# Kernel optimization log

Measured on AMD Instinct MI355X. Metric: run time of the kernel, lower is better.

The kernel has to match this reference:

```python
import jax, jax.numpy as jnp
import numpy as np

K = 3  # kernel_size
P = K * K  # patch length per channel


def setup_inputs() -> dict:
    key = jax.random.key(0)
    k1, k2 = jax.random.split(key)
    B, H, W, C_in, C_out = 16, 64, 64, 64, 64
    L = P * (P + 1) // 2 + P + 1  # 45 quadratic + 9 linear + 1 bias = 55
    x = jax.random.normal(k1, (B, H, W, C_in), dtype=jnp.float32)
    # glorot-ish scale for the flat kernel [1,1,L,C_in,C_out]
    flat_kernel = jax.random.normal(k2, (1, 1, L, C_in, C_out), dtype=jnp.float32) * 0.05
    return {"x": x, "flat_kernel": flat_kernel}


def _quadratic_features(x):
    # x: [B,H,W,C] NHWC; stride 1, 'same' padding, k=3
    B, H, W, C = x.shape
    pad = K // 2
    xp = jnp.pad(x, ((0, 0), (pad, pad), (pad, pad), (0, 0)))
    # patches: [B,H,W,P,C] -- loop is over the 9 fixed kernel taps only
    patches = jnp.stack(
        [xp[:, i:i + H, j:j + W, :] for i in range(K) for j in range(K)], axis=3
    )
    iu, ju = np.triu_indices(P)  # all pairs i<=j incl. squares -> 45 terms
    quad = patches[:, :, :, iu, :] * patches[:, :, :, ju, :]  # [B,H,W,45,C]
    ones = jnp.ones_like(patches[:, :, :, :1, :])              # bias term
    # flat features per the use_linear_and_bias=True layout: [quad | linear | 1]
    return jnp.concatenate([quad, patches, ones], axis=3)       # [B,H,W,55,C]


def reference(x, flat_kernel):
    feats = _quadratic_features(x)          # [B,H,W,L,C]
    w = flat_kernel[0, 0]                   # [L,C,O]
    # contract over flat-feature index L and input channels C
    return jnp.einsum('bhwlc,lco->bhwo', feats, w)
```

## Files before the change

### kernel.cpp

```cpp
#include <hip/hip_runtime.h>

typedef _Float16 half8 __attribute__((ext_vector_type(8)));
typedef _Float16 half4v __attribute__((ext_vector_type(4)));
typedef float f32x16 __attribute__((ext_vector_type(16)));

#define BOFF 0
#define XOFF 110592
#define LDS_TOTAL 152832

__device__ __forceinline__ void stage16(const void* g, const void* l) {
  __builtin_amdgcn_global_load_lds(
      (const __attribute__((address_space(1))) unsigned int*)(unsigned long long)g,
      (__attribute__((address_space(3))) unsigned int*)(unsigned int)(unsigned long long)l,
      16, 0, 0);
}

__global__ __launch_bounds__(256)
void prepack_kernel(const float* __restrict__ W, _Float16* __restrict__ Bp) {
  const int idx = blockIdx.x * 256 + threadIdx.x;
  if (idx < 221184) {
    const int v   = idx & 7;
    const int lam = (idx >> 3) & 63;
    const int f   = idx >> 9;
    const int l   = f % 54;
    const int r   = f / 54;
    const int cc  = r & 1;
    const int ks  = (r >> 1) & 1;
    const int nt  = (r >> 2) & 1;
    const int c   = (ks * 2 + cc) * 16 + (lam >> 5) * 8 + v;
    const int o   = nt * 32 + (lam & 31);
    Bp[idx] = (_Float16)W[(l * 64 + c) * 64 + o];
  } else if (idx < 221184 + 64) {
    const int o = idx - 221184;
    float s = 0.f;
    for (int c = 0; c < 64; ++c) s += W[(54 * 64 + c) * 64 + o];
    ((float*)(Bp + 221184))[o] = s;
  }
}

__global__ __launch_bounds__(512, 2)
void qconv_kernel(const float* __restrict__ x, const _Float16* __restrict__ Bp,
                  float* __restrict__ out) {
  constexpr int IU[45] = {0,0,0,0,0,0,0,0,0, 1,1,1,1,1,1,1,1, 2,2,2,2,2,2,2,
                          3,3,3,3,3,3, 4,4,4,4,4, 5,5,5,5, 6,6,6, 7,7, 8};
  constexpr int JU[45] = {0,1,2,3,4,5,6,7,8, 1,2,3,4,5,6,7,8, 2,3,4,5,6,7,8,
                          3,4,5,6,7,8, 4,5,6,7,8, 5,6,7,8, 6,7,8, 7,8, 8};

  const int tid  = threadIdx.x;
  const int wave = tid >> 6;
  const int lane = tid & 63;
  const int colA = lane & 31;
  const int kg   = lane >> 5;

  const int phys = blockIdx.x;
  const int xcd  = phys & 7;
  const int slot = phys >> 3;
  const int g    = xcd * 16 + (slot >> 1);
  const int nt   = slot & 1;
  const int b    = g >> 3;
  const int r0   = (g & 7) * 8;

  __shared__ __align__(16) unsigned char smem[LDS_TOTAL];
  const char* BpB = (const char*)Bp;

  f32x16 acc[2] = {};

  for (int ks = 0; ks < 2; ++ks) {
    __syncthreads();

    const size_t bSrc = (size_t)(nt * 2 + ks) * 110592;
    for (int f = wave; f < 108; f += 8)
      stage16(BpB + bSrc + (size_t)f * 1024 + lane * 16,
              (char*)smem + BOFF + f * 1024);

    for (int idx = tid; idx < 5280; idx += 512) {
      const int row = idx / 528;
      const int rem = idx - row * 528;
      const int col = rem >> 3;
      const int gq  = rem & 7;
      const int hh  = r0 - 1 + row;
      const int ww  = col - 1;
      float4 v = make_float4(0.f, 0.f, 0.f, 0.f);
      if ((unsigned)hh < 64u && (unsigned)ww < 64u)
        v = *(const float4*)(x + ((((size_t)b * 64 + hh) * 64 + ww) * 64
                                  + ks * 32 + gq * 4));
      half4v hv;
      hv[0] = (_Float16)v.x; hv[1] = (_Float16)v.y;
      hv[2] = (_Float16)v.z; hv[3] = (_Float16)v.w;
      const int addr = XOFF + ((row * 4224 + col * 64 + gq * 8)
                               ^ (((col >> 1) & 3) << 4));
      *(half4v*)(smem + addr) = hv;
    }

    asm volatile("s_waitcnt vmcnt(0)" ::: "memory");
    __syncthreads();

#pragma unroll
    for (int cc = 0; cc < 2; ++cc) {
      half8 tap[2][9];
#pragma unroll
      for (int mt = 0; mt < 2; ++mt)
#pragma unroll
        for (int t = 0; t < 9; ++t) {
          const int xrow = wave + t / 3;
          const int ce   = mt * 32 + colA + (t % 3);
          const int a = XOFF + ((xrow * 4224 + ce * 64 + cc * 32 + kg * 16)
                                ^ (((ce >> 1) & 3) << 4));
          tap[mt][t] = *(const half8*)(smem + a);
        }

      const unsigned fb = BOFF + cc * 54 * 1024 + lane * 16;
      half8 pfA = *(const half8*)(smem + fb);
      half8 pfB = *(const half8*)(smem + fb + 1024);
#pragma unroll
      for (int l = 0; l < 54; ++l) {
        const half8 bf = (l & 1) ? pfB : pfA;
        if (l + 2 < 54) {
          if (l & 1) pfB = *(const half8*)(smem + fb + (l + 2) * 1024);
          else       pfA = *(const half8*)(smem + fb + (l + 2) * 1024);
        }
#pragma unroll
        for (int mt = 0; mt < 2; ++mt) {
          half8 a;
          if (l < 45) a = tap[mt][IU[l]] * tap[mt][JU[l]];
          else        a = tap[mt][l - 45];
          acc[mt] = __builtin_amdgcn_mfma_f32_32x32x16_f16(a, bf, acc[mt],
                                                           0, 0, 0);
        }
      }
    }
  }

  const float bias = ((const float*)(BpB + 442368))[nt * 32 + colA];
#pragma unroll
  for (int mt = 0; mt < 2; ++mt) {
    float* op = out + (((size_t)b * 64 + r0 + wave) * 64 + mt * 32) * 64
                    + nt * 32 + colA;
#pragma unroll
    for (int gi = 0; gi < 16; ++gi) {
      const int rowD = (gi & 3) + 8 * (gi >> 2) + 4 * kg;
      op[(size_t)rowD * 64] = acc[mt][gi] + bias;
    }
  }
}

extern "C" void kernel_launch(void* const* d_in, const int* in_sizes, int n_in,
                              void* d_out, int out_size, void* d_ws, size_t ws_size,
                              hipStream_t stream) {
  const float* x = (const float*)d_in[0];
  const float* W = (const float*)d_in[1];
  float* out     = (float*)d_out;
  _Float16* Bp   = (_Float16*)d_ws;

  prepack_kernel<<<dim3((221248 + 255) / 256), dim3(256), 0, stream>>>(W, Bp);
  qconv_kernel<<<dim3(256), dim3(512), 0, stream>>>(x, Bp, out);
}
```

Baseline: 40.61 us.

## Double-buffer weight slices in LDS and load input taps directly from global

Splits the reduction into four channel-chunk phases, each staging only one 54-row weight slice into one of two LDS slots. The next slice is prefetched asynchronously while the current one is consumed, with a single barrier per phase. The LDS staging of the input halo tile is removed: each lane reads its 9 taps straight from global memory as float4 pairs and converts them to half in registers, and weight reads are prefetched eight deep. This cuts LDS use and barrier stalls, but adds redundant global reads of overlapping taps across lanes and waves, and more register pressure.

Result: slower. 61.58 us (+51.6%).

```diff
diff --git a/kernel.cpp b/kernel.cpp
--- a/kernel.cpp
+++ b/kernel.cpp
@@ -1,12 +1,10 @@
 #include <hip/hip_runtime.h>
 
 typedef _Float16 half8 __attribute__((ext_vector_type(8)));
-typedef _Float16 half4v __attribute__((ext_vector_type(4)));
 typedef float f32x16 __attribute__((ext_vector_type(16)));
 
-#define BOFF 0
-#define XOFF 110592
-#define LDS_TOTAL 152832
+#define SLOT 55296
+#define LDS_TOTAL (2 * SLOT)
 
 __device__ __forceinline__ void stage16(const void* g, const void* l) {
   __builtin_amdgcn_global_load_lds(
@@ -59,82 +57,97 @@
   const int nt   = slot & 1;
   const int b    = g >> 3;
   const int r0   = (g & 7) * 8;
+  const int r    = r0 + wave;
 
   __shared__ __align__(16) unsigned char smem[LDS_TOTAL];
   const char* BpB = (const char*)Bp;
 
+  {
+    const size_t src = (size_t)((nt * 2 + 0) * 2 + 0) * SLOT;
+#pragma unroll
+    for (int q = 0; q < 7; ++q) {
+      const int f = min(wave * 7 + q, 53);
+      stage16(BpB + src + (size_t)f * 1024 + lane * 16,
+              (char*)smem + 0 * SLOT + f * 1024);
+    }
+  }
+  __syncthreads();
+
   f32x16 acc[2] = {};
 
-  for (int ks = 0; ks < 2; ++ks) {
-    __syncthreads();
+  for (int p = 0; p < 4; ++p) {
+    const int ks = p >> 1;
+    const int cc = p & 1;
+    const int chb = (ks * 2 + cc) * 16 + kg * 8;
 
-    const size_t bSrc = (size_t)(nt * 2 + ks) * 110592;
-    for (int f = wave; f < 108; f += 8)
-      stage16(BpB + bSrc + (size_t)f * 1024 + lane * 16,
-              (char*)smem + BOFF + f * 1024);
-
-    for (int idx = tid; idx < 5280; idx += 512) {
-      const int row = idx / 528;
-      const int rem = idx - row * 528;
-      const int col = rem >> 3;
-      const int gq  = rem & 7;
-      const int hh  = r0 - 1 + row;
-      const int ww  = col - 1;
-      float4 v = make_float4(0.f, 0.f, 0.f, 0.f);
-      if ((unsigned)hh < 64u && (unsigned)ww < 64u)
-        v = *(const float4*)(x + ((((size_t)b * 64 + hh) * 64 + ww) * 64
-                                  + ks * 32 + gq * 4));
-      half4v hv;
-      hv[0] = (_Float16)v.x; hv[1] = (_Float16)v.y;
-      hv[2] = (_Float16)v.z; hv[3] = (_Float16)v.w;
-      const int addr = XOFF + ((row * 4224 + col * 64 + gq * 8)
-                               ^ (((col >> 1) & 3) << 4));
-      *(half4v*)(smem + addr) = hv;
+    half8 tap[2][9];
+#pragma unroll
+    for (int mt = 0; mt < 2; ++mt) {
+      float4 tlo[9], thi[9];
+#pragma unroll
+      for (int t = 0; t < 9; ++t) {
+        const int rr = r + t / 3 - 1;
+        const int cl = mt * 32 + colA + (t % 3) - 1;
+        float4 z = make_float4(0.f, 0.f, 0.f, 0.f);
+        tlo[t] = z; thi[t] = z;
+        if ((unsigned)rr < 64u && (unsigned)cl < 64u) {
+          const float* pa = x + ((((size_t)b * 64 + rr) * 64 + cl) * 64 + chb);
+          tlo[t] = *(const float4*)pa;
+          thi[t] = *(const float4*)(pa + 4);
+        }
+      }
+#pragma unroll
+      for (int t = 0; t < 9; ++t) {
+        half8 hv;
+        hv[0] = (_Float16)tlo[t].x; hv[1] = (_Float16)tlo[t].y;
+        hv[2] = (_Float16)tlo[t].z; hv[3] = (_Float16)tlo[t].w;
+        hv[4] = (_Float16)thi[t].x; hv[5] = (_Float16)thi[t].y;
+        hv[6] = (_Float16)thi[t].z; hv[7] = (_Float16)thi[t].w;
+        tap[mt][t] = hv;
+      }
     }
 
-    asm volatile("s_waitcnt vmcnt(0)" ::: "memory");
-    __syncthreads();
-
+    asm volatile("" ::: "memory");
+    if (p < 3) {
+      const int pn = p + 1;
+      const size_t src = (size_t)((nt * 2 + (pn >> 1)) * 2 + (pn & 1)) * SLOT;
 #pragma unroll
-    for (int cc = 0; cc < 2; ++cc) {
-      half8 tap[2][9];
-#pragma unroll
-      for (int mt = 0; mt < 2; ++mt)
-#pragma unroll
-        for (int t = 0; t < 9; ++t) {
-          const int xrow = wave + t / 3;
-          const int ce   = mt * 32 + colA + (t % 3);
-          const int a = XOFF + ((xrow * 4224 + ce * 64 + cc * 32 + kg * 16)
-                                ^ (((ce >> 1) & 3) << 4));
-          tap[mt][t] = *(const half8*)(smem + a);
-        }
-
-      const unsigned fb = BOFF + cc * 54 * 1024 + lane * 16;
-      half8 pfA = *(const half8*)(smem + fb);
-      half8 pfB = *(const half8*)(smem + fb + 1024);
-#pragma unroll
-      for (int l = 0; l < 54; ++l) {
-        const half8 bf = (l & 1) ? pfB : pfA;
-        if (l + 2 < 54) {
-          if (l & 1) pfB = *(const half8*)(smem + fb + (l + 2) * 1024);
-          else       pfA = *(const half8*)(smem + fb + (l + 2) * 1024);
-        }
-#pragma unroll
-        for (int mt = 0; mt < 2; ++mt) {
-          half8 a;
-          if (l < 45) a = tap[mt][IU[l]] * tap[mt][JU[l]];
-          else        a = tap[mt][l - 45];
-          acc[mt] = __builtin_amdgcn_mfma_f32_32x32x16_f16(a, bf, acc[mt],
-                                                           0, 0, 0);
-        }
+      for (int q = 0; q < 7; ++q) {
+        const int f = min(wave * 7 + q, 53);
+        stage16(BpB + src + (size_t)f * 1024 + lane * 16,
+                (char*)smem + (pn & 1) * SLOT + f * 1024);
       }
     }
+
+    const unsigned sbase = (p & 1) * SLOT + lane * 16;
+    half8 bq[8];
+#pragma unroll
+    for (int q = 0; q < 8; ++q)
+      bq[q] = *(const half8*)(smem + sbase + q * 1024);
+#pragma unroll
+    for (int l = 0; l < 54; ++l) {
+      const half8 bf = bq[l & 7];
+      if (l + 8 < 54)
+        bq[l & 7] = *(const half8*)(smem + sbase + (l + 8) * 1024);
+      half8 a0, a1;
+      if (l < 45) {
+        a0 = tap[0][IU[l]] * tap[0][JU[l]];
+        a1 = tap[1][IU[l]] * tap[1][JU[l]];
+      } else {
+        a0 = tap[0][l - 45];
+        a1 = tap[1][l - 45];
+      }
+      acc[0] = __builtin_amdgcn_mfma_f32_32x32x16_f16(a0, bf, acc[0], 0, 0, 0);
+      acc[1] = __builtin_amdgcn_mfma_f32_32x32x16_f16(a1, bf, acc[1], 0, 0, 0);
+    }
+
+    __syncthreads();
   }
 
   const float bias = ((const float*)(BpB + 442368))[nt * 32 + colA];
 #pragma unroll
   for (int mt = 0; mt < 2; ++mt) {
-    float* op = out + (((size_t)b * 64 + r0 + wave) * 64 + mt * 32) * 64
+    float* op = out + (((size_t)b * 64 + r) * 64 + mt * 32) * 64
                     + nt * 32 + colA;
 #pragma unroll
     for (int gi = 0; gi < 16; ++gi) {
```

## Software-pipeline LDS loads of weights and taps across MFMA groups

Applied to the files above, without the earlier changes.

Restructures the inner compute into groups of nine MFMA steps with double-buffered weight fragments loaded a group ahead. The second channel-chunk's tap loads are spread across the first chunk's MFMA groups, and s_setprio is raised around MFMA bursts. The aim is to hide LDS latency behind matrix ops. In exchange it holds many more live half8 values in registers, which risks spills under the 2-blocks-per-CU launch bound.

Result: slower. 55.96 us (+37.8%).

```diff
diff --git a/kernel.cpp b/kernel.cpp
--- a/kernel.cpp
+++ b/kernel.cpp
@@ -64,6 +64,54 @@
   const char* BpB = (const char*)Bp;
 
   f32x16 acc[2] = {};
+  half8 bqE[9], bqO[9];
+  half8 tapA[2][9], tapB[2][9];
+
+#define TAPLOAD(tp, cc)                                                     \
+  _Pragma("unroll")                                                         \
+  for (int mt = 0; mt < 2; ++mt)                                            \
+    _Pragma("unroll")                                                       \
+    for (int t = 0; t < 9; ++t) {                                           \
+      const int xrow = wave + t / 3;                                        \
+      const int ce   = mt * 32 + colA + (t % 3);                            \
+      const int aa = XOFF + ((xrow * 4224 + ce * 64 + (cc) * 32 + kg * 16)  \
+                             ^ (((ce >> 1) & 3) << 4));                     \
+      tp[mt][t] = *(const half8*)(smem + aa);                               \
+    }
+
+#define LOADQ(buf, cc, p)                                                   \
+  _Pragma("unroll")                                                         \
+  for (int q = 0; q < 9; ++q)                                               \
+    buf[q] = *(const half8*)(smem + BOFF + (cc) * 55296 +                   \
+                             ((p) * 9 + q) * 1024 + lane * 16);
+
+#define TRICK(p)                                                            \
+  _Pragma("unroll")                                                         \
+  for (int j = 0; j < 3; ++j) {                                             \
+    const int q  = (p) * 3 + j;                                             \
+    const int mt = q / 9, tt = q % 9;                                       \
+    const int xrow = wave + tt / 3;                                         \
+    const int ce   = mt * 32 + colA + (tt % 3);                             \
+    const int aa = XOFF + ((xrow * 4224 + ce * 64 + 32 + kg * 16)           \
+                           ^ (((ce >> 1) & 3) << 4));                       \
+    tapB[mt][tt] = *(const half8*)(smem + aa);                              \
+  }
+
+#define MFMA9(tp, buf, l0)                                                  \
+  __builtin_amdgcn_s_setprio(1);                                            \
+  _Pragma("unroll")                                                         \
+  for (int q = 0; q < 9; ++q) {                                             \
+    const int l = (l0) + q;                                                 \
+    half8 a0, a1;                                                           \
+    if (l < 45) { a0 = tp[0][IU[l]] * tp[0][JU[l]];                         \
+                  a1 = tp[1][IU[l]] * tp[1][JU[l]]; }                       \
+    else        { a0 = tp[0][l - 45]; a1 = tp[1][l - 45]; }                 \
+    acc[0] = __builtin_amdgcn_mfma_f32_32x32x16_f16(a0, buf[q], acc[0],     \
+                                                    0, 0, 0);               \
+    acc[1] = __builtin_amdgcn_mfma_f32_32x32x16_f16(a1, buf[q], acc[1],     \
+                                                    0, 0, 0);               \
+  }                                                                         \
+  __builtin_amdgcn_s_setprio(0);
 
   for (int ks = 0; ks < 2; ++ks) {
     __syncthreads();
@@ -95,40 +143,20 @@
     asm volatile("s_waitcnt vmcnt(0)" ::: "memory");
     __syncthreads();
 
-#pragma unroll
-    for (int cc = 0; cc < 2; ++cc) {
-      half8 tap[2][9];
-#pragma unroll
-      for (int mt = 0; mt < 2; ++mt)
-#pragma unroll
-        for (int t = 0; t < 9; ++t) {
-          const int xrow = wave + t / 3;
-          const int ce   = mt * 32 + colA + (t % 3);
-          const int a = XOFF + ((xrow * 4224 + ce * 64 + cc * 32 + kg * 16)
-                                ^ (((ce >> 1) & 3) << 4));
-          tap[mt][t] = *(const half8*)(smem + a);
-        }
-
-      const unsigned fb = BOFF + cc * 54 * 1024 + lane * 16;
-      half8 pfA = *(const half8*)(smem + fb);
-      half8 pfB = *(const half8*)(smem + fb + 1024);
-#pragma unroll
-      for (int l = 0; l < 54; ++l) {
-        const half8 bf = (l & 1) ? pfB : pfA;
-        if (l + 2 < 54) {
-          if (l & 1) pfB = *(const half8*)(smem + fb + (l + 2) * 1024);
-          else       pfA = *(const half8*)(smem + fb + (l + 2) * 1024);
-        }
-#pragma unroll
-        for (int mt = 0; mt < 2; ++mt) {
-          half8 a;
-          if (l < 45) a = tap[mt][IU[l]] * tap[mt][JU[l]];
-          else        a = tap[mt][l - 45];
-          acc[mt] = __builtin_amdgcn_mfma_f32_32x32x16_f16(a, bf, acc[mt],
-                                                           0, 0, 0);
-        }
-      }
-    }
+    TAPLOAD(tapA, 0);
+    LOADQ(bqE, 0, 0);
+    LOADQ(bqO, 0, 1);  TRICK(0);  MFMA9(tapA, bqE, 0);
+    LOADQ(bqE, 0, 2);  TRICK(1);  MFMA9(tapA, bqO, 9);
+    LOADQ(bqO, 0, 3);  TRICK(2);  MFMA9(tapA, bqE, 18);
+    LOADQ(bqE, 0, 4);  TRICK(3);  MFMA9(tapA, bqO, 27);
+    LOADQ(bqO, 0, 5);  TRICK(4);  MFMA9(tapA, bqE, 36);
+    LOADQ(bqE, 1, 0);  TRICK(5);  MFMA9(tapA, bqO, 45);
+    LOADQ(bqO, 1, 1);  MFMA9(tapB, bqE, 0);
+    LOADQ(bqE, 1, 2);  MFMA9(tapB, bqO, 9);
+    LOADQ(bqO, 1, 3);  MFMA9(tapB, bqE, 18);
+    LOADQ(bqE, 1, 4);  MFMA9(tapB, bqO, 27);
+    LOADQ(bqO, 1, 5);  MFMA9(tapB, bqE, 36);
+                       MFMA9(tapB, bqO, 45);
   }
 
   const float bias = ((const float*)(BpB + 442368))[nt * 32 + colA];
```

## Halve block size, stage weights per channel chunk, and batch LDS loads around MFMA groups

Applied to the files above, without the earlier changes.

The grid doubles to 512 blocks of 256 threads, each covering 4 output rows instead of 8, and LDS use drops to about 80 KB so two blocks can share a CU. Weights are now staged one 32-channel chunk at a time across four phases instead of two. The x tile is reloaded only when the input-channel half changes. The inner loop loads weight fragments in groups of six, double-buffered, and raises wave priority around each MFMA burst to overlap LDS reads with matrix work. The cost is more barriers and global weight traffic per output row, plus a larger halo overhead from the smaller row tiles.

Result: slower. 42.33 us (+4.2%).

```diff
diff --git a/kernel.cpp b/kernel.cpp
--- a/kernel.cpp
+++ b/kernel.cpp
@@ -5,8 +5,8 @@
 typedef float f32x16 __attribute__((ext_vector_type(16)));
 
 #define BOFF 0
-#define XOFF 110592
-#define LDS_TOTAL 152832
+#define XOFF 55296
+#define LDS_TOTAL 80640
 
 __device__ __forceinline__ void stage16(const void* g, const void* l) {
   __builtin_amdgcn_global_load_lds(
@@ -38,7 +38,7 @@
   }
 }
 
-__global__ __launch_bounds__(512, 2)
+__global__ __launch_bounds__(256, 2)
 void qconv_kernel(const float* __restrict__ x, const _Float16* __restrict__ Bp,
                   float* __restrict__ out) {
   constexpr int IU[45] = {0,0,0,0,0,0,0,0,0, 1,1,1,1,1,1,1,1, 2,2,2,2,2,2,2,
@@ -53,88 +53,102 @@
   const int kg   = lane >> 5;
 
   const int phys = blockIdx.x;
-  const int xcd  = phys & 7;
-  const int slot = phys >> 3;
-  const int g    = xcd * 16 + (slot >> 1);
-  const int nt   = slot & 1;
-  const int b    = g >> 3;
-  const int r0   = (g & 7) * 8;
+  const int logical = (phys & 7) * 64 + (phys >> 3);
+  const int nt  = logical & 1;
+  const int grp = logical >> 1;
+  const int b   = grp >> 4;
+  const int r0  = (grp & 15) * 4;
+  const int r   = r0 + wave;
 
   __shared__ __align__(16) unsigned char smem[LDS_TOTAL];
   const char* BpB = (const char*)Bp;
 
   f32x16 acc[2] = {};
+  half8 tap[2][9];
+  half8 bqE[6], bqO[6];
 
-  for (int ks = 0; ks < 2; ++ks) {
+#define LOADQ(buf, p)                                                       \
+  _Pragma("unroll")                                                         \
+  for (int q = 0; q < 6; ++q)                                               \
+    buf[q] = *(const half8*)(smem + BOFF + ((p) * 6 + q) * 1024 + lane * 16);
+
+#define MFMA6(buf, l0)                                                      \
+  __builtin_amdgcn_s_setprio(1);                                            \
+  _Pragma("unroll")                                                         \
+  for (int q = 0; q < 6; ++q) {                                             \
+    const int l = (l0) + q;                                                 \
+    half8 a0, a1;                                                           \
+    if (l < 45) { a0 = tap[0][IU[l]] * tap[0][JU[l]];                       \
+                  a1 = tap[1][IU[l]] * tap[1][JU[l]]; }                     \
+    else        { a0 = tap[0][l - 45]; a1 = tap[1][l - 45]; }               \
+    acc[0] = __builtin_amdgcn_mfma_f32_32x32x16_f16(a0, buf[q], acc[0],     \
+                                                    0, 0, 0);               \
+    acc[1] = __builtin_amdgcn_mfma_f32_32x32x16_f16(a1, buf[q], acc[1],     \
+                                                    0, 0, 0);               \
+  }                                                                         \
+  __builtin_amdgcn_s_setprio(0);
+
+  for (int p = 0; p < 4; ++p) {
+    const int ks = p >> 1;
+    const int cc = p & 1;
     __syncthreads();
 
-    const size_t bSrc = (size_t)(nt * 2 + ks) * 110592;
-    for (int f = wave; f < 108; f += 8)
-      stage16(BpB + bSrc + (size_t)f * 1024 + lane * 16,
+    const size_t bsrc = (size_t)(((nt * 2 + ks) * 2 + cc) * 54) * 1024;
+    for (int f = wave; f < 54; f += 4)
+      stage16(BpB + bsrc + (size_t)f * 1024 + lane * 16,
               (char*)smem + BOFF + f * 1024);
 
-    for (int idx = tid; idx < 5280; idx += 512) {
-      const int row = idx / 528;
-      const int rem = idx - row * 528;
-      const int col = rem >> 3;
-      const int gq  = rem & 7;
-      const int hh  = r0 - 1 + row;
-      const int ww  = col - 1;
-      float4 v = make_float4(0.f, 0.f, 0.f, 0.f);
-      if ((unsigned)hh < 64u && (unsigned)ww < 64u)
-        v = *(const float4*)(x + ((((size_t)b * 64 + hh) * 64 + ww) * 64
-                                  + ks * 32 + gq * 4));
-      half4v hv;
-      hv[0] = (_Float16)v.x; hv[1] = (_Float16)v.y;
-      hv[2] = (_Float16)v.z; hv[3] = (_Float16)v.w;
-      const int addr = XOFF + ((row * 4224 + col * 64 + gq * 8)
-                               ^ (((col >> 1) & 3) << 4));
-      *(half4v*)(smem + addr) = hv;
+    if (cc == 0) {
+      for (int idx = tid; idx < 3168; idx += 256) {
+        const int row = idx / 528;
+        const int rem = idx - row * 528;
+        const int col = rem >> 3;
+        const int gq  = rem & 7;
+        const int hh  = r0 - 1 + row;
+        const int ww  = col - 1;
+        float4 v = make_float4(0.f, 0.f, 0.f, 0.f);
+        if ((unsigned)hh < 64u && (unsigned)ww < 64u)
+          v = *(const float4*)(x + ((((size_t)b * 64 + hh) * 64 + ww) * 64
+                                    + ks * 32 + gq * 4));
+        half4v hv;
+        hv[0] = (_Float16)v.x; hv[1] = (_Float16)v.y;
+        hv[2] = (_Float16)v.z; hv[3] = (_Float16)v.w;
+        const int addr = XOFF + ((row * 4224 + col * 64 + gq * 8)
+                                 ^ (((col >> 1) & 3) << 4));
+        *(half4v*)(smem + addr) = hv;
+      }
     }
 
     asm volatile("s_waitcnt vmcnt(0)" ::: "memory");
     __syncthreads();
 
 #pragma unroll
-    for (int cc = 0; cc < 2; ++cc) {
-      half8 tap[2][9];
+    for (int mt = 0; mt < 2; ++mt)
 #pragma unroll
-      for (int mt = 0; mt < 2; ++mt)
-#pragma unroll
-        for (int t = 0; t < 9; ++t) {
-          const int xrow = wave + t / 3;
-          const int ce   = mt * 32 + colA + (t % 3);
-          const int a = XOFF + ((xrow * 4224 + ce * 64 + cc * 32 + kg * 16)
-                                ^ (((ce >> 1) & 3) << 4));
-          tap[mt][t] = *(const half8*)(smem + a);
-        }
+      for (int t = 0; t < 9; ++t) {
+        const int xrow = wave + t / 3;
+        const int ce   = mt * 32 + colA + (t % 3);
+        const int aa = XOFF + ((xrow * 4224 + ce * 64 + cc * 32 + kg * 16)
+                               ^ (((ce >> 1) & 3) << 4));
+        tap[mt][t] = *(const half8*)(smem + aa);
+      }
 
-      const unsigned fb = BOFF + cc * 54 * 1024 + lane * 16;
-      half8 pfA = *(const half8*)(smem + fb);
-      half8 pfB = *(const half8*)(smem + fb + 1024);
-#pragma unroll
-      for (int l = 0; l < 54; ++l) {
-        const half8 bf = (l & 1) ? pfB : pfA;
-        if (l + 2 < 54) {
-          if (l & 1) pfB = *(const half8*)(smem + fb + (l + 2) * 1024);
-          else       pfA = *(const half8*)(smem + fb + (l + 2) * 1024);
-        }
-#pragma unroll
-        for (int mt = 0; mt < 2; ++mt) {
-          half8 a;
-          if (l < 45) a = tap[mt][IU[l]] * tap[mt][JU[l]];
-          else        a = tap[mt][l - 45];
-          acc[mt] = __builtin_amdgcn_mfma_f32_32x32x16_f16(a, bf, acc[mt],
-                                                           0, 0, 0);
-        }
-      }
-    }
+    LOADQ(bqE, 0);
+    LOADQ(bqO, 1);  MFMA6(bqE, 0);
+    LOADQ(bqE, 2);  MFMA6(bqO, 6);
+    LOADQ(bqO, 3);  MFMA6(bqE, 12);
+    LOADQ(bqE, 4);  MFMA6(bqO, 18);
+    LOADQ(bqO, 5);  MFMA6(bqE, 24);
+    LOADQ(bqE, 6);  MFMA6(bqO, 30);
+    LOADQ(bqO, 7);  MFMA6(bqE, 36);
+    LOADQ(bqE, 8);  MFMA6(bqO, 42);
+                    MFMA6(bqE, 48);
   }
 
   const float bias = ((const float*)(BpB + 442368))[nt * 32 + colA];
 #pragma unroll
   for (int mt = 0; mt < 2; ++mt) {
-    float* op = out + (((size_t)b * 64 + r0 + wave) * 64 + mt * 32) * 64
+    float* op = out + (((size_t)b * 64 + r) * 64 + mt * 32) * 64
                     + nt * 32 + colA;
 #pragma unroll
     for (int gi = 0; gi < 16; ++gi) {
@@ -153,5 +167,5 @@
   _Float16* Bp   = (_Float16*)d_ws;
 
   prepack_kernel<<<dim3((221248 + 255) / 256), dim3(256), 0, stream>>>(W, Bp);
-  qconv_kernel<<<dim3(256), dim3(512), 0, stream>>>(x, Bp, out);
+  qconv_kernel<<<dim3(512), dim3(256), 0, stream>>>(x, Bp, out);
 }
```
